# Kernel tuning notes

Hardware: AMD Instinct MI355X
Metric: run time of the kernel (lower is better)

The kernel has to match this reference:

```python
import jax, jax.numpy as jnp
import numpy as np

B, C, H, W = 4, 96, 64, 64
D_STATE, D_CONV, EXPAND = 16, 4, 2
D_INNER = EXPAND * C          # 192
DT_RANK = (C + 15) // 16      # 6
BN_EPS = 1e-5


def setup_inputs() -> dict:
    key = jax.random.key(0)
    ks = jax.random.split(key, 10)
    s = 0.02
    return {
        "x": jax.random.normal(ks[0], (B, C, H, W), jnp.float32),
        # Mamba block params (mamba_ssm layout, no bias on in/out proj)
        "in_proj_w": jax.random.normal(ks[1], (2 * D_INNER, C), jnp.float32) * s,
        "conv1d_w": jax.random.normal(ks[2], (D_INNER, 1, D_CONV), jnp.float32) * s,  # depthwise
        "conv1d_b": jnp.zeros((D_INNER,), jnp.float32),
        "x_proj_w": jax.random.normal(ks[3], (DT_RANK + 2 * D_STATE, D_INNER), jnp.float32) * s,
        "dt_proj_w": jax.random.normal(ks[4], (D_INNER, DT_RANK), jnp.float32) * s,
        "dt_proj_b": jax.random.normal(ks[5], (D_INNER,), jnp.float32) * s,
        "A_log": jnp.log(jnp.tile(jnp.arange(1, D_STATE + 1, dtype=jnp.float32), (D_INNER, 1))),
        "D": jnp.ones((D_INNER,), jnp.float32),
        "out_proj_w": jax.random.normal(ks[6], (C, D_INNER), jnp.float32) * s,
        # trailing ConvBNReLU6 params
        "conv2d_w": jax.random.normal(ks[7], (C, C, 3, 3), jnp.float32) * s,
        "bn_gamma": jnp.ones((C,), jnp.float32),
        "bn_beta": jnp.zeros((C,), jnp.float32),
        "bn_mean": jnp.zeros((C,), jnp.float32),
        "bn_var": jnp.ones((C,), jnp.float32),
    }


def _forward(x, in_proj_w, conv1d_w, conv1d_b, x_proj_w, dt_proj_w, dt_proj_b,
             A_log, D, out_proj_w, conv2d_w, bn_gamma, bn_beta, bn_mean, bn_var):
    b, c, h, w = x.shape
    L = h * w
    seq = x.reshape(b, c, L).transpose(0, 2, 1)              # [B, L, C] tokens
    xz = seq @ in_proj_w.T                                    # [B, L, 2*D_INNER]
    xi, z = jnp.split(xz, 2, axis=-1)

    # depthwise causal conv1d + SiLU
    xi_c = jax.lax.conv_general_dilated(
        xi.transpose(0, 2, 1), conv1d_w, (1,), [(D_CONV - 1, 0)],
        dimension_numbers=("NCH", "OIH", "NCH"), feature_group_count=D_INNER)
    xi = jax.nn.silu((xi_c + conv1d_b[None, :, None]).transpose(0, 2, 1))  # [B, L, D_INNER]

    # input-dependent dt, B, C
    x_dbl = xi @ x_proj_w.T                                   # [B, L, DT_RANK + 2*D_STATE]
    dt, Bm, Cm = jnp.split(x_dbl, [DT_RANK, DT_RANK + D_STATE], axis=-1)
    dt = jax.nn.softplus(dt @ dt_proj_w.T + dt_proj_b)        # [B, L, D_INNER]

    # discretize: dA = exp(dt*A), dBx = dt*B*x
    A = -jnp.exp(A_log)                                       # [D_INNER, D_STATE]
    dA = jnp.exp(dt[..., None] * A)                           # [B, L, D_INNER, D_STATE]
    dBx = dt[..., None] * Bm[:, :, None, :] * xi[..., None]   # [B, L, D_INNER, D_STATE]

    def step(hst, inputs):
        dA_t, dBx_t, C_t = inputs
        hst = dA_t * hst + dBx_t                              # [B, D_INNER, D_STATE]
        y_t = jnp.einsum("bds,bs->bd", hst, C_t)
        return hst, y_t

    h0 = jnp.zeros((b, D_INNER, D_STATE), xi.dtype)
    _, ys = jax.lax.scan(step, h0,
                         (dA.transpose(1, 0, 2, 3), dBx.transpose(1, 0, 2, 3), Cm.transpose(1, 0, 2)))
    y = ys.transpose(1, 0, 2)                                 # [B, L, D_INNER]
    y = (y + xi * D) * jax.nn.silu(z)                         # skip D + gate
    out = y @ out_proj_w.T                                    # [B, L, C]
    xm = out.transpose(0, 2, 1).reshape(b, c, h, w)

    # ConvBNReLU: 3x3 conv (pad 1, no bias) -> BN (inference) -> ReLU6
    xo = jax.lax.conv_general_dilated(xm, conv2d_w, (1, 1), [(1, 1), (1, 1)],
                                      dimension_numbers=("NCHW", "OIHW", "NCHW"))
    inv = bn_gamma / jnp.sqrt(bn_var + BN_EPS)
    xo = xo * inv[None, :, None, None] + (bn_beta - bn_mean * inv)[None, :, None, None]
    return jnp.clip(xo, 0.0, 6.0)


def reference(x, in_proj_w, conv1d_w, conv1d_b, x_proj_w, dt_proj_w, dt_proj_b,
              A_log, D, out_proj_w, conv2d_w, bn_gamma, bn_beta, bn_mean, bn_var):
    return _forward(x, in_proj_w, conv1d_w, conv1d_b, x_proj_w, dt_proj_w, dt_proj_b,
                    A_log, D, out_proj_w, conv2d_w, bn_gamma, bn_beta, bn_mean, bn_var)
```

## Files before the change

kernel.cpp:

```cpp
#include <hip/hip_runtime.h>
#include <math.h>

#define LQ 4096
#define DI 192
#define DS 16
#define NCH 128
#define TCH 32

__device__ __forceinline__ float siluf_(float v) { return v / (1.f + __expf(-v)); }
__device__ __forceinline__ float softplusf_(float v) { return v > 20.f ? v : log1pf(__expf(v)); }

template <int CTRL>
__device__ __forceinline__ float dpp_shift_(float x) {
    int y = __builtin_amdgcn_update_dpp(0, __float_as_int(x), CTRL, 0xf, 0xf, true);
    return __int_as_float(y);
}
__device__ __forceinline__ void async_g2l16_(const float* g, float* l) {
    __builtin_amdgcn_global_load_lds(
        (const __attribute__((address_space(1))) void*)g,
        (__attribute__((address_space(3))) void*)l, 16, 0, 0);
}
__device__ __forceinline__ void async_g2l4_(const float* g, float* l) {
    __builtin_amdgcn_global_load_lds(
        (const __attribute__((address_space(1))) void*)g,
        (__attribute__((address_space(3))) void*)l, 4, 0, 0);
}

__global__ __launch_bounds__(256) void k1_inproj(const float* __restrict__ x,
    const float* __restrict__ w, float* __restrict__ xi_raw, float* __restrict__ z)
{
    const int l0 = blockIdx.x * 64;
    const int n0 = blockIdx.y * 64;
    const int b  = blockIdx.z;
    __shared__ float xs[96 * 64];
    __shared__ float wsT[96 * 68];
    const int tid = threadIdx.x;
    for (int i = tid; i < 96 * 16; i += 256) {
        int c = i >> 4, lq = i & 15;
        *(float4*)&xs[c * 64 + lq * 4] =
            *(const float4*)&x[(b * 96 + c) * LQ + l0 + lq * 4];
    }
    for (int i = tid; i < 64 * 24; i += 256) {
        int n = i / 24, cq = i - n * 24;
        float4 v = *(const float4*)&w[(n0 + n) * 96 + cq * 4];
        wsT[(cq * 4 + 0) * 68 + n] = v.x;
        wsT[(cq * 4 + 1) * 68 + n] = v.y;
        wsT[(cq * 4 + 2) * 68 + n] = v.z;
        wsT[(cq * 4 + 3) * 68 + n] = v.w;
    }
    __syncthreads();
    const int tx = tid & 15;
    const int ty = tid >> 4;
    float acc[4][4];
#pragma unroll
    for (int i = 0; i < 4; ++i)
#pragma unroll
        for (int j = 0; j < 4; ++j) acc[i][j] = 0.f;
    for (int k = 0; k < 96; ++k) {
        float4 a  = *(const float4*)&xs[k * 64 + ty * 4];
        float4 bb = *(const float4*)&wsT[k * 68 + tx * 4];
        float av[4] = {a.x, a.y, a.z, a.w};
        float bv[4] = {bb.x, bb.y, bb.z, bb.w};
#pragma unroll
        for (int i = 0; i < 4; ++i)
#pragma unroll
            for (int j = 0; j < 4; ++j) acc[i][j] += av[i] * bv[j];
    }
    float* dst = (n0 < DI) ? xi_raw : z;
    const int nn0 = (n0 < DI) ? n0 : (n0 - DI);
#pragma unroll
    for (int i = 0; i < 4; ++i) {
        int l = l0 + ty * 4 + i;
        float4 v = make_float4(acc[i][0], acc[i][1], acc[i][2], acc[i][3]);
        *(float4*)&dst[(b * LQ + l) * DI + nn0 + tx * 4] = v;
    }
}

__global__ __launch_bounds__(256) void k2_conv1d(const float* __restrict__ xir,
    const float* __restrict__ cw, const float* __restrict__ cb, float* __restrict__ xi)
{
    int idx = blockIdx.x * 256 + threadIdx.x;
    int d = idx % DI;
    int l = (idx / DI) & (LQ - 1);
    float4 wv = *(const float4*)&cw[d * 4];
    float wk[4] = {wv.x, wv.y, wv.z, wv.w};
    float acc = cb[d];
#pragma unroll
    for (int k = 0; k < 4; ++k) {
        int lp = l - 3 + k;
        if (lp >= 0) acc += wk[k] * xir[idx + (k - 3) * DI];
    }
    xi[idx] = siluf_(acc);
}

__global__ __launch_bounds__(256) void k3_xdbl(const float* __restrict__ xi,
    const float* __restrict__ xw, float* __restrict__ xdbl)
{
    const int l0 = blockIdx.x * 64;
    const int b  = blockIdx.y;
    __shared__ float sxiT[96 * 68];
    __shared__ float swx[38 * 196];
    const int tid = threadIdx.x;
    for (int i = tid; i < 38 * 48; i += 256) {
        int n = i / 48, kq = i - n * 48;
        *(float4*)&swx[n * 196 + kq * 4] = *(const float4*)&xw[n * 192 + kq * 4];
    }
    const int lq = tid & 15, ng = tid >> 4;
    float acc[3][4];
#pragma unroll
    for (int p = 0; p < 3; ++p)
#pragma unroll
        for (int i = 0; i < 4; ++i) acc[p][i] = 0.f;
    for (int half = 0; half < 2; ++half) {
        __syncthreads();
        for (int i = tid; i < 64 * 24; i += 256) {
            int l = i / 24, kq = i - l * 24;
            float4 v = *(const float4*)&xi[(b * LQ + l0 + l) * DI + half * 96 + kq * 4];
            sxiT[(kq * 4 + 0) * 68 + l] = v.x;
            sxiT[(kq * 4 + 1) * 68 + l] = v.y;
            sxiT[(kq * 4 + 2) * 68 + l] = v.z;
            sxiT[(kq * 4 + 3) * 68 + l] = v.w;
        }
        __syncthreads();
#pragma unroll
        for (int pass = 0; pass < 3; ++pass) {
            int n = pass * 16 + ng;
            if (n >= 38) continue;
            for (int k = 0; k < 96; ++k) {
                float4 a = *(const float4*)&sxiT[k * 68 + lq * 4];
                float bv = swx[n * 196 + half * 96 + k];
                acc[pass][0] += a.x * bv;
                acc[pass][1] += a.y * bv;
                acc[pass][2] += a.z * bv;
                acc[pass][3] += a.w * bv;
            }
        }
    }
#pragma unroll
    for (int pass = 0; pass < 3; ++pass) {
        int n = pass * 16 + ng;
        if (n >= 38) continue;
#pragma unroll
        for (int i = 0; i < 4; ++i)
            xdbl[(b * LQ + l0 + lq * 4 + i) * 38 + n] = acc[pass][i];
    }
}

__global__ __launch_bounds__(192) void k4_scanA(
    const float* __restrict__ xdbl, const float* __restrict__ xi,
    const float* __restrict__ dtw, const float* __restrict__ dtb,
    const float* __restrict__ alog,
    float* __restrict__ cA, float* __restrict__ cB)
{
    const int ch = blockIdx.x, b = blockIdx.y;
    const int t0 = ch * TCH;
    __shared__ float sxd[TCH * 40];
    const int d = threadIdx.x;
    for (int i = d; i < TCH * 38; i += 192) {
        int t = i / 38, cc = i - t * 38;
        sxd[t * 40 + cc] = xdbl[(b * LQ + t0 + t) * 38 + cc];
    }
    float dtw6[6];
#pragma unroll
    for (int r = 0; r < 6; ++r) dtw6[r] = dtw[d * 6 + r];
    const float dtbd = dtb[d];
    float Ads[16];
#pragma unroll
    for (int s = 0; s < 16; ++s) Ads[s] = -__expf(alog[d * 16 + s]);
    float a[16], hb[16];
#pragma unroll
    for (int s = 0; s < 16; ++s) { a[s] = 1.f; hb[s] = 0.f; }
    __syncthreads();
    float xiv_next = xi[(b * LQ + t0) * DI + d];
    for (int t = 0; t < TCH; ++t) {
        float xiv = xiv_next;
        if (t + 1 < TCH) xiv_next = xi[(b * LQ + t0 + t + 1) * DI + d];
        float acc = dtbd;
#pragma unroll
        for (int r = 0; r < 6; ++r) acc = fmaf(sxd[t * 40 + r], dtw6[r], acc);
        float dtv = softplusf_(acc);
        float dtxi = dtv * xiv;
        const float* Bp = &sxd[t * 40 + 6];
#pragma unroll
        for (int s = 0; s < 16; ++s) {
            float dA = __expf(dtv * Ads[s]);
            a[s] *= dA;
            hb[s] = fmaf(dA, hb[s], dtxi * Bp[s]);
        }
    }
    int o = ((b * NCH + ch) * DI + d) * 16;
#pragma unroll
    for (int s = 0; s < 16; s += 4) {
        *(float4*)&cA[o + s] = make_float4(a[s], a[s + 1], a[s + 2], a[s + 3]);
        *(float4*)&cB[o + s] = make_float4(hb[s], hb[s + 1], hb[s + 2], hb[s + 3]);
    }
}

__global__ __launch_bounds__(256) void k5_combine(const float* cA,
    const float* __restrict__ cB, float* hinit)
{
    int gid = blockIdx.x * 256 + threadIdx.x;
    int b = gid / 3072;
    int rem = gid - b * 3072;
    int base = b * (NCH * 3072) + rem;
    float h = 0.f;
#pragma unroll 8
    for (int c = 0; c < NCH; ++c) {
        int o = base + c * 3072;
        float av = cA[o];
        float bv = cB[o];
        hinit[o] = h;
        h = fmaf(av, h, bv);
    }
}

__global__ __launch_bounds__(192) void k6_scanC(
    const float* __restrict__ xdbl, const float* __restrict__ xi,
    const float* __restrict__ z, const float* __restrict__ dtw,
    const float* __restrict__ dtb, const float* __restrict__ alog,
    const float* __restrict__ Dp, const float* __restrict__ hinit,
    float* __restrict__ yg)
{
    const int ch = blockIdx.x, b = blockIdx.y;
    const int t0 = ch * TCH;
    __shared__ float sxd[TCH * 40];
    const int d = threadIdx.x;
    for (int i = d; i < TCH * 38; i += 192) {
        int t = i / 38, cc = i - t * 38;
        sxd[t * 40 + cc] = xdbl[(b * LQ + t0 + t) * 38 + cc];
    }
    float dtw6[6];
#pragma unroll
    for (int r = 0; r < 6; ++r) dtw6[r] = dtw[d * 6 + r];
    const float dtbd = dtb[d];
    const float Dd = Dp[d];
    float Ads[16];
#pragma unroll
    for (int s = 0; s < 16; ++s) Ads[s] = -__expf(alog[d * 16 + s]);
    float h[16];
    const int o = ((b * NCH + ch) * DI + d) * 16;
#pragma unroll
    for (int s = 0; s < 16; s += 4) {
        float4 v = *(const float4*)&hinit[o + s];
        h[s] = v.x; h[s + 1] = v.y; h[s + 2] = v.z; h[s + 3] = v.w;
    }
    __syncthreads();
    float xiv_next = xi[(b * LQ + t0) * DI + d];
    float zv_next  = z[(b * LQ + t0) * DI + d];
    for (int t = 0; t < TCH; ++t) {
        float xiv = xiv_next, zv = zv_next;
        if (t + 1 < TCH) {
            xiv_next = xi[(b * LQ + t0 + t + 1) * DI + d];
            zv_next  = z[(b * LQ + t0 + t + 1) * DI + d];
        }
        float acc = dtbd;
#pragma unroll
        for (int r = 0; r < 6; ++r) acc = fmaf(sxd[t * 40 + r], dtw6[r], acc);
        float dtv = softplusf_(acc);
        float dtxi = dtv * xiv;
        const float* Bp = &sxd[t * 40 + 6];
        const float* Cp = &sxd[t * 40 + 22];
        float y0 = 0.f, y1 = 0.f, y2 = 0.f, y3 = 0.f;
#pragma unroll
        for (int s = 0; s < 16; s += 4) {
            float dA0 = __expf(dtv * Ads[s]);
            float dA1 = __expf(dtv * Ads[s + 1]);
            float dA2 = __expf(dtv * Ads[s + 2]);
            float dA3 = __expf(dtv * Ads[s + 3]);
            h[s]     = fmaf(dA0, h[s],     dtxi * Bp[s]);
            h[s + 1] = fmaf(dA1, h[s + 1], dtxi * Bp[s + 1]);
            h[s + 2] = fmaf(dA2, h[s + 2], dtxi * Bp[s + 2]);
            h[s + 3] = fmaf(dA3, h[s + 3], dtxi * Bp[s + 3]);
            y0 = fmaf(h[s],     Cp[s],     y0);
            y1 = fmaf(h[s + 1], Cp[s + 1], y1);
            y2 = fmaf(h[s + 2], Cp[s + 2], y2);
            y3 = fmaf(h[s + 3], Cp[s + 3], y3);
        }
        float y = (y0 + y1) + (y2 + y3);
        float gate = siluf_(zv);
        yg[(b * LQ + t0 + t) * DI + d] = (y + xiv * Dd) * gate;
    }
}

__global__ __launch_bounds__(256) void k7_outproj(const float* __restrict__ yg,
    const float* __restrict__ wo, float* __restrict__ xm)
{
    const int l0 = blockIdx.x * 64;
    const int n0 = blockIdx.y * 32;
    const int b  = blockIdx.z;
    __shared__ float syT[96 * 68];
    __shared__ float wtT[192 * 36];
    const int tid = threadIdx.x;
    for (int i = tid; i < 32 * 48; i += 256) {
        int n = i / 48, kq = i - n * 48;
        float4 v = *(const float4*)&wo[(n0 + n) * DI + kq * 4];
        wtT[(kq * 4 + 0) * 36 + n] = v.x;
        wtT[(kq * 4 + 1) * 36 + n] = v.y;
        wtT[(kq * 4 + 2) * 36 + n] = v.z;
        wtT[(kq * 4 + 3) * 36 + n] = v.w;
    }
    const int tx = tid & 15;
    const int ty = tid >> 4;
    float acc[2][4];
#pragma unroll
    for (int j = 0; j < 2; ++j)
#pragma unroll
        for (int i = 0; i < 4; ++i) acc[j][i] = 0.f;
    for (int half = 0; half < 2; ++half) {
        __syncthreads();
        for (int i = tid; i < 64 * 24; i += 256) {
            int l = i / 24, kq = i - l * 24;
            float4 v = *(const float4*)&yg[(b * LQ + l0 + l) * DI + half * 96 + kq * 4];
            syT[(kq * 4 + 0) * 68 + l] = v.x;
            syT[(kq * 4 + 1) * 68 + l] = v.y;
            syT[(kq * 4 + 2) * 68 + l] = v.z;
            syT[(kq * 4 + 3) * 68 + l] = v.w;
        }
        __syncthreads();
        for (int k = 0; k < 96; ++k) {
            float4 a = *(const float4*)&syT[k * 68 + tx * 4];
            int kk = half * 96 + k;
            float b0 = wtT[kk * 36 + ty * 2 + 0];
            float b1 = wtT[kk * 36 + ty * 2 + 1];
            acc[0][0] += a.x * b0; acc[0][1] += a.y * b0;
            acc[0][2] += a.z * b0; acc[0][3] += a.w * b0;
            acc[1][0] += a.x * b1; acc[1][1] += a.y * b1;
            acc[1][2] += a.z * b1; acc[1][3] += a.w * b1;
        }
    }
#pragma unroll
    for (int j = 0; j < 2; ++j) {
        float4 v = make_float4(acc[j][0], acc[j][1], acc[j][2], acc[j][3]);
        *(float4*)&xm[(b * 96 + n0 + ty * 2 + j) * LQ + l0 + tx * 4] = v;
    }
}

#define K8_INQ 384
#define K8_WNEL 576
__global__ __launch_bounds__(256) void k8_conv3(const float* __restrict__ xm,
    const float* __restrict__ w2, float* __restrict__ pbuf)
{
    const int ks  = blockIdx.x & 3;
    const int co0 = (blockIdx.x >> 2) * 16;
    const int y0  = blockIdx.y * 4;
    const int b   = blockIdx.z;
    __shared__ float sin2[2][1536];
    __shared__ float swt2[2][576];
    const int tid = threadIdx.x;
    const int sx = tid & 15;
    const int sy = (tid >> 4) & 3;
    const int cq = tid >> 6;

    int in_goff[2];
    bool in_ok[2];
#pragma unroll
    for (int j = 0; j < 2; ++j) {
        int i = tid + j * 256;
        int ci  = i / 96;
        int rem = i - ci * 96;
        int row = rem >> 4;
        int qx  = rem & 15;
        int gy  = y0 + row - 1;
        bool ok = (i < K8_INQ) && gy >= 0 && gy < 64;
        in_ok[j]  = ok;
        in_goff[j] = ok ? (ci * 4096 + gy * 64 + qx * 4) : 0;
    }
    int w_goff[3];
#pragma unroll
    for (int j = 0; j < 3; ++j) {
        int i = tid + j * 256;
        int ci  = i / 144;
        int rem = i - ci * 144;
        int k   = rem >> 4;
        int cl  = rem & 15;
        w_goff[j] = (i < K8_WNEL) ? (cl * 864 + ci * 9 + k) : 0;
    }

    const float* xb = xm + (size_t)b * 96 * 4096 + (size_t)ks * 24 * 4096;
    const float* wb = w2 + (size_t)co0 * 864 + ks * 24 * 9;
    const float4 zero4 = make_float4(0.f, 0.f, 0.f, 0.f);

#pragma unroll
    for (int bu = 0; bu < 2; ++bu) {
        if (!in_ok[0]) *(float4*)&sin2[bu][tid * 4] = zero4;
        if (tid < 128 && !in_ok[1]) *(float4*)&sin2[bu][(256 + tid) * 4] = zero4;
    }

    {
        const float* gx = xb;
        const float* gw = wb;
        if (in_ok[0]) async_g2l16_(gx + in_goff[0], &sin2[0][cq * 256]);
        if (tid < 128 && in_ok[1]) async_g2l16_(gx + in_goff[1], &sin2[0][1024 + cq * 256]);
        async_g2l4_(gw + w_goff[0], &swt2[0][cq * 64]);
        async_g2l4_(gw + w_goff[1], &swt2[0][256 + cq * 64]);
        if (tid < 64) async_g2l4_(gw + w_goff[2], &swt2[0][512 + cq * 64]);
    }
    __syncthreads();

    float acc[4][4];
#pragma unroll
    for (int c = 0; c < 4; ++c)
#pragma unroll
        for (int x = 0; x < 4; ++x) acc[c][x] = 0.f;

#pragma clang loop unroll(disable)
    for (int ch = 0; ch < 6; ++ch) {
        if (ch < 5) {
            const int nb = (ch + 1) & 1;
            const float* gx = xb + (ch + 1) * 16384;
            const float* gw = wb + (ch + 1) * 36;
            if (in_ok[0]) async_g2l16_(gx + in_goff[0], &sin2[nb][cq * 256]);
            if (tid < 128 && in_ok[1]) async_g2l16_(gx + in_goff[1], &sin2[nb][1024 + cq * 256]);
            async_g2l4_(gw + w_goff[0], &swt2[nb][cq * 64]);
            async_g2l4_(gw + w_goff[1], &swt2[nb][256 + cq * 64]);
            if (tid < 64) async_g2l4_(gw + w_goff[2], &swt2[nb][512 + cq * 64]);
        }

        const float* sc = sin2[ch & 1];
        const float* wc = swt2[ch & 1];
#pragma unroll
        for (int cii = 0; cii < 4; ++cii) {
            float w6[3][6];
#pragma unroll
            for (int r = 0; r < 3; ++r) {
                float4 v = *(const float4*)&sc[(cii * 6 + sy + r) * 64 + sx * 4];
                w6[r][0] = dpp_shift_<0x111>(v.w);
                w6[r][1] = v.x; w6[r][2] = v.y; w6[r][3] = v.z; w6[r][4] = v.w;
                w6[r][5] = dpp_shift_<0x101>(v.x);
            }
#pragma unroll
            for (int ky = 0; ky < 3; ++ky) {
#pragma unroll
                for (int kx = 0; kx < 3; ++kx) {
                    float4 wv = *(const float4*)&wc[(cii * 9 + ky * 3 + kx) * 16 + cq * 4];
#pragma unroll
                    for (int x = 0; x < 4; ++x) {
                        float pv = w6[ky][x + kx];
                        acc[0][x] = fmaf(pv, wv.x, acc[0][x]);
                        acc[1][x] = fmaf(pv, wv.y, acc[1][x]);
                        acc[2][x] = fmaf(pv, wv.z, acc[2][x]);
                        acc[3][x] = fmaf(pv, wv.w, acc[3][x]);
                    }
                }
            }
        }
        __syncthreads();
    }

    const int yy = y0 + sy;
    float* pb = pbuf + (size_t)ks * 1572864;
#pragma unroll
    for (int c = 0; c < 4; ++c) {
        const int cc = co0 + cq * 4 + c;
        float4 o = make_float4(acc[c][0], acc[c][1], acc[c][2], acc[c][3]);
        *(float4*)&pb[((size_t)(b * 96 + cc) * 64 + yy) * 64 + sx * 4] = o;
    }
}

__global__ __launch_bounds__(256) void k9_reduce(const float* __restrict__ pbuf,
    const float* __restrict__ bng, const float* __restrict__ bnb,
    const float* __restrict__ bnm, const float* __restrict__ bnv,
    float* __restrict__ out)
{
    const int q = blockIdx.x * 256 + threadIdx.x;
    const int idx = q * 4;
    const int c = (idx >> 12) % 96;
    float4 s = *(const float4*)&pbuf[idx];
    float4 s1 = *(const float4*)&pbuf[idx + 1572864];
    float4 s2 = *(const float4*)&pbuf[idx + 2 * 1572864];
    float4 s3 = *(const float4*)&pbuf[idx + 3 * 1572864];
    s.x += s1.x + s2.x + s3.x;
    s.y += s1.y + s2.y + s3.y;
    s.z += s1.z + s2.z + s3.z;
    s.w += s1.w + s2.w + s3.w;
    float inv = bng[c] / sqrtf(bnv[c] + 1e-5f);
    float add = bnb[c] - bnm[c] * inv;
    float4 o;
    o.x = fminf(fmaxf(s.x * inv + add, 0.f), 6.f);
    o.y = fminf(fmaxf(s.y * inv + add, 0.f), 6.f);
    o.z = fminf(fmaxf(s.z * inv + add, 0.f), 6.f);
    o.w = fminf(fmaxf(s.w * inv + add, 0.f), 6.f);
    *(float4*)&out[idx] = o;
}

extern "C" void kernel_launch(void* const* d_in, const int* in_sizes, int n_in,
                              void* d_out, int out_size, void* d_ws, size_t ws_size,
                              hipStream_t stream) {
    (void)in_sizes; (void)n_in; (void)out_size; (void)ws_size;
    const float* x    = (const float*)d_in[0];
    const float* w_in = (const float*)d_in[1];
    const float* cw   = (const float*)d_in[2];
    const float* cb   = (const float*)d_in[3];
    const float* xw   = (const float*)d_in[4];
    const float* dtw  = (const float*)d_in[5];
    const float* dtb  = (const float*)d_in[6];
    const float* alog = (const float*)d_in[7];
    const float* Dp   = (const float*)d_in[8];
    const float* wo   = (const float*)d_in[9];
    const float* w2   = (const float*)d_in[10];
    const float* bng  = (const float*)d_in[11];
    const float* bnb  = (const float*)d_in[12];
    const float* bnm  = (const float*)d_in[13];
    const float* bnv  = (const float*)d_in[14];

    float* ws = (float*)d_ws;
    float* xi_raw = ws;
    float* z      = ws + 3145728;
    float* xi     = ws + 6291456;
    float* xdbl   = ws + 9437184;
    float* cA     = ws + 10059776;
    float* cB     = ws + 11632640;
    float* hinit  = cA;
    float* xm     = cB;
    float* yg     = xi_raw;
    float* pbuf   = xi_raw;

    dim3 blk(256);
    k1_inproj<<<dim3(64, 6, 4), blk, 0, stream>>>(x, w_in, xi_raw, z);
    k2_conv1d<<<dim3(12288), blk, 0, stream>>>(xi_raw, cw, cb, xi);
    k3_xdbl<<<dim3(64, 4), blk, 0, stream>>>(xi, xw, xdbl);
    k4_scanA<<<dim3(NCH, 4), dim3(192), 0, stream>>>(xdbl, xi, dtw, dtb, alog, cA, cB);
    k5_combine<<<dim3(48), blk, 0, stream>>>(cA, cB, hinit);
    k6_scanC<<<dim3(NCH, 4), dim3(192), 0, stream>>>(xdbl, xi, z, dtw, dtb, alog, Dp, hinit, yg);
    k7_outproj<<<dim3(64, 3, 4), blk, 0, stream>>>(yg, wo, xm);
    k8_conv3<<<dim3(24, 16, 4), blk, 0, stream>>>(xm, w2, pbuf);
    k9_reduce<<<dim3(1536), blk, 0, stream>>>(pbuf, bng, bnb, bnm, bnv, (float*)d_out);
}
```

Measured before the change: 292.6 us.

## Split SSM state dimension across thread pairs in chunked scan kernels

```diff
diff --git a/kernel.cpp b/kernel.cpp
--- a/kernel.cpp
+++ b/kernel.cpp
@@ -10,6 +10,11 @@
 __device__ __forceinline__ float siluf_(float v) { return v / (1.f + __expf(-v)); }
 __device__ __forceinline__ float softplusf_(float v) { return v > 20.f ? v : log1pf(__expf(v)); }
 
+template <int CTRL>
+__device__ __forceinline__ float dpp_add_(float x) {
+    int y = __builtin_amdgcn_update_dpp(0, __float_as_int(x), CTRL, 0xf, 0xf, true);
+    return x + __int_as_float(y);
+}
 template <int CTRL>
 __device__ __forceinline__ float dpp_shift_(float x) {
     int y = __builtin_amdgcn_update_dpp(0, __float_as_int(x), CTRL, 0xf, 0xf, true);
@@ -146,7 +151,7 @@
     }
 }
 
-__global__ __launch_bounds__(192) void k4_scanA(
+__global__ __launch_bounds__(384) void k4_scanA(
     const float* __restrict__ xdbl, const float* __restrict__ xi,
     const float* __restrict__ dtw, const float* __restrict__ dtb,
     const float* __restrict__ alog,
@@ -154,22 +159,24 @@
 {
     const int ch = blockIdx.x, b = blockIdx.y;
     const int t0 = ch * TCH;
-    __shared__ float sxd[TCH * 40];
-    const int d = threadIdx.x;
-    for (int i = d; i < TCH * 38; i += 192) {
+    __shared__ float sxd[TCH * 48];
+    const int tid = threadIdx.x;
+    const int d = tid >> 1, sg = tid & 1;
+    for (int i = tid; i < TCH * 38; i += 384) {
         int t = i / 38, cc = i - t * 38;
-        sxd[t * 40 + cc] = xdbl[(b * LQ + t0 + t) * 38 + cc];
+        int slot = cc + (cc >= 6 ? 2 : 0);
+        sxd[t * 48 + slot] = xdbl[(b * LQ + t0 + t) * 38 + cc];
     }
     float dtw6[6];
 #pragma unroll
     for (int r = 0; r < 6; ++r) dtw6[r] = dtw[d * 6 + r];
     const float dtbd = dtb[d];
-    float Ads[16];
-#pragma unroll
-    for (int s = 0; s < 16; ++s) Ads[s] = -__expf(alog[d * 16 + s]);
-    float a[16], hb[16];
-#pragma unroll
-    for (int s = 0; s < 16; ++s) { a[s] = 1.f; hb[s] = 0.f; }
+    float Ads[8];
+#pragma unroll
+    for (int s = 0; s < 8; ++s) Ads[s] = -__expf(alog[d * 16 + sg * 8 + s]);
+    float a[8], hb[8];
+#pragma unroll
+    for (int s = 0; s < 8; ++s) { a[s] = 1.f; hb[s] = 0.f; }
     __syncthreads();
     float xiv_next = xi[(b * LQ + t0) * DI + d];
     for (int t = 0; t < TCH; ++t) {
@@ -177,20 +184,23 @@
         if (t + 1 < TCH) xiv_next = xi[(b * LQ + t0 + t + 1) * DI + d];
         float acc = dtbd;
 #pragma unroll
-        for (int r = 0; r < 6; ++r) acc = fmaf(sxd[t * 40 + r], dtw6[r], acc);
+        for (int r = 0; r < 6; ++r) acc = fmaf(sxd[t * 48 + r], dtw6[r], acc);
         float dtv = softplusf_(acc);
         float dtxi = dtv * xiv;
-        const float* Bp = &sxd[t * 40 + 6];
-#pragma unroll
-        for (int s = 0; s < 16; ++s) {
+        const float* Bp = &sxd[t * 48 + 8 + sg * 8];
+        float4 B0 = *(const float4*)Bp;
+        float4 B1 = *(const float4*)(Bp + 4);
+        float Bv[8] = {B0.x, B0.y, B0.z, B0.w, B1.x, B1.y, B1.z, B1.w};
+#pragma unroll
+        for (int s = 0; s < 8; ++s) {
             float dA = __expf(dtv * Ads[s]);
             a[s] *= dA;
-            hb[s] = fmaf(dA, hb[s], dtxi * Bp[s]);
-        }
-    }
-    int o = ((b * NCH + ch) * DI + d) * 16;
-#pragma unroll
-    for (int s = 0; s < 16; s += 4) {
+            hb[s] = fmaf(dA, hb[s], dtxi * Bv[s]);
+        }
+    }
+    int o = ((b * NCH + ch) * DI + d) * 16 + sg * 8;
+#pragma unroll
+    for (int s = 0; s < 8; s += 4) {
         *(float4*)&cA[o + s] = make_float4(a[s], a[s + 1], a[s + 2], a[s + 3]);
         *(float4*)&cB[o + s] = make_float4(hb[s], hb[s + 1], hb[s + 2], hb[s + 3]);
     }
@@ -214,7 +224,7 @@
     }
 }
 
-__global__ __launch_bounds__(192) void k6_scanC(
+__global__ __launch_bounds__(384) void k6_scanC(
     const float* __restrict__ xdbl, const float* __restrict__ xi,
     const float* __restrict__ z, const float* __restrict__ dtw,
     const float* __restrict__ dtb, const float* __restrict__ alog,
@@ -223,24 +233,26 @@
 {
     const int ch = blockIdx.x, b = blockIdx.y;
     const int t0 = ch * TCH;
-    __shared__ float sxd[TCH * 40];
-    const int d = threadIdx.x;
-    for (int i = d; i < TCH * 38; i += 192) {
+    __shared__ float sxd[TCH * 48];
+    const int tid = threadIdx.x;
+    const int d = tid >> 1, sg = tid & 1;
+    for (int i = tid; i < TCH * 38; i += 384) {
         int t = i / 38, cc = i - t * 38;
-        sxd[t * 40 + cc] = xdbl[(b * LQ + t0 + t) * 38 + cc];
+        int slot = cc + (cc >= 6 ? 2 : 0);
+        sxd[t * 48 + slot] = xdbl[(b * LQ + t0 + t) * 38 + cc];
     }
     float dtw6[6];
 #pragma unroll
     for (int r = 0; r < 6; ++r) dtw6[r] = dtw[d * 6 + r];
     const float dtbd = dtb[d];
     const float Dd = Dp[d];
-    float Ads[16];
-#pragma unroll
-    for (int s = 0; s < 16; ++s) Ads[s] = -__expf(alog[d * 16 + s]);
-    float h[16];
-    const int o = ((b * NCH + ch) * DI + d) * 16;
-#pragma unroll
-    for (int s = 0; s < 16; s += 4) {
+    float Ads[8];
+#pragma unroll
+    for (int s = 0; s < 8; ++s) Ads[s] = -__expf(alog[d * 16 + sg * 8 + s]);
+    float h[8];
+    const int o = ((b * NCH + ch) * DI + d) * 16 + sg * 8;
+#pragma unroll
+    for (int s = 0; s < 8; s += 4) {
         float4 v = *(const float4*)&hinit[o + s];
         h[s] = v.x; h[s + 1] = v.y; h[s + 2] = v.z; h[s + 3] = v.w;
     }
@@ -255,30 +267,32 @@
         }
         float acc = dtbd;
 #pragma unroll
-        for (int r = 0; r < 6; ++r) acc = fmaf(sxd[t * 40 + r], dtw6[r], acc);
+        for (int r = 0; r < 6; ++r) acc = fmaf(sxd[t * 48 + r], dtw6[r], acc);
         float dtv = softplusf_(acc);
         float dtxi = dtv * xiv;
-        const float* Bp = &sxd[t * 40 + 6];
-        const float* Cp = &sxd[t * 40 + 22];
-        float y0 = 0.f, y1 = 0.f, y2 = 0.f, y3 = 0.f;
-#pragma unroll
-        for (int s = 0; s < 16; s += 4) {
+        const float* Bp = &sxd[t * 48 + 8 + sg * 8];
+        const float* Cp = &sxd[t * 48 + 24 + sg * 8];
+        float4 B0 = *(const float4*)Bp;
+        float4 B1 = *(const float4*)(Bp + 4);
+        float4 C0 = *(const float4*)Cp;
+        float4 C1 = *(const float4*)(Cp + 4);
+        float Bv[8] = {B0.x, B0.y, B0.z, B0.w, B1.x, B1.y, B1.z, B1.w};
+        float Cv[8] = {C0.x, C0.y, C0.z, C0.w, C1.x, C1.y, C1.z, C1.w};
+        float y0 = 0.f, y1 = 0.f;
+#pragma unroll
+        for (int s = 0; s < 8; s += 2) {
             float dA0 = __expf(dtv * Ads[s]);
             float dA1 = __expf(dtv * Ads[s + 1]);
-            float dA2 = __expf(dtv * Ads[s + 2]);
-            float dA3 = __expf(dtv * Ads[s + 3]);
-            h[s]     = fmaf(dA0, h[s],     dtxi * Bp[s]);
-            h[s + 1] = fmaf(dA1, h[s + 1], dtxi * Bp[s + 1]);
-            h[s + 2] = fmaf(dA2, h[s + 2], dtxi * Bp[s + 2]);
-            h[s + 3] = fmaf(dA3, h[s + 3], dtxi * Bp[s + 3]);
-            y0 = fmaf(h[s],     Cp[s],     y0);
-            y1 = fmaf(h[s + 1], Cp[s + 1], y1);
-            y2 = fmaf(h[s + 2], Cp[s + 2], y2);
-            y3 = fmaf(h[s + 3], Cp[s + 3], y3);
-        }
-        float y = (y0 + y1) + (y2 + y3);
-        float gate = siluf_(zv);
-        yg[(b * LQ + t0 + t) * DI + d] = (y + xiv * Dd) * gate;
+            h[s]     = fmaf(dA0, h[s],     dtxi * Bv[s]);
+            h[s + 1] = fmaf(dA1, h[s + 1], dtxi * Bv[s + 1]);
+            y0 = fmaf(h[s],     Cv[s],     y0);
+            y1 = fmaf(h[s + 1], Cv[s + 1], y1);
+        }
+        float y = dpp_add_<0xB1>(y0 + y1);
+        if (sg == 0) {
+            float gate = siluf_(zv);
+            yg[(b * LQ + t0 + t) * DI + d] = (y + xiv * Dd) * gate;
+        }
     }
 }
 
@@ -519,9 +533,9 @@
     k1_inproj<<<dim3(64, 6, 4), blk, 0, stream>>>(x, w_in, xi_raw, z);
     k2_conv1d<<<dim3(12288), blk, 0, stream>>>(xi_raw, cw, cb, xi);
     k3_xdbl<<<dim3(64, 4), blk, 0, stream>>>(xi, xw, xdbl);
-    k4_scanA<<<dim3(NCH, 4), dim3(192), 0, stream>>>(xdbl, xi, dtw, dtb, alog, cA, cB);
+    k4_scanA<<<dim3(NCH, 4), dim3(384), 0, stream>>>(xdbl, xi, dtw, dtb, alog, cA, cB);
     k5_combine<<<dim3(48), blk, 0, stream>>>(cA, cB, hinit);
-    k6_scanC<<<dim3(NCH, 4), dim3(192), 0, stream>>>(xdbl, xi, z, dtw, dtb, alog, Dp, hinit, yg);
+    k6_scanC<<<dim3(NCH, 4), dim3(384), 0, stream>>>(xdbl, xi, z, dtw, dtb, alog, Dp, hinit, yg);
     k7_outproj<<<dim3(64, 3, 4), blk, 0, stream>>>(yg, wo, xm);
     k8_conv3<<<dim3(24, 16, 4), blk, 0, stream>>>(xm, w2, pbuf);
     k9_reduce<<<dim3(1536), blk, 0, stream>>>(pbuf, bng, bnb, bnm, bnv, (float*)d_out);
```

Result: slower. 314.5 us (+7.5%).
